# Kernel tuning notes

Measured on AMD Instinct MI355X. Metric: run time of the kernel, lower is better.

## Reference

```python
import jax, jax.numpy as jnp
import numpy as np

B, DIM, X, Y = 2, 256, 48, 48
HEADS, DIM_HEAD = 8, 64
DIM_INNER = HEADS * DIM_HEAD
MASK_SELF_VALUE = -100.0
EPS = 1e-12


def setup_inputs() -> dict:
    key = jax.random.key(0)
    k0, k1, k2, k3, k4 = jax.random.split(key, 5)
    return {
        "fmap": jax.random.normal(k0, (B, DIM, X, Y), dtype=jnp.float32),
        "gamma": jnp.ones((DIM,), dtype=jnp.float32),
        "w_qk": jax.random.normal(k1, (DIM_INNER, DIM), dtype=jnp.float32) * 0.02,
        "w_v": jax.random.normal(k2, (DIM_INNER, DIM), dtype=jnp.float32) * 0.02,
        "null_kv": jax.random.normal(k3, (2, HEADS, DIM_HEAD), dtype=jnp.float32),
        "w_out": jax.random.normal(k4, (DIM, DIM_INNER), dtype=jnp.float32) * 0.02,
    }


def _safe_sqrt(d2):
    # matches torch.cdist subgradient: zero grad at zero distance
    pos = d2 > 0
    return jnp.where(pos, jnp.sqrt(jnp.where(pos, d2, 1.0)), 0.0)


def reference(fmap, gamma, w_qk, w_v, null_kv, w_out):
    b, c, x, y = fmap.shape
    h, dh = HEADS, DIM_HEAD
    n = x * y
    scale = dh ** -0.5

    # ChannelRMSNorm: L2-normalize over channel dim, * sqrt(dim) * gamma
    l2 = jnp.sqrt(jnp.sum(fmap * fmap, axis=1, keepdims=True))
    normed = fmap / jnp.maximum(l2, EPS) * jnp.sqrt(jnp.float32(c)) * gamma[None, :, None, None]

    flat = normed.reshape(b, c, n)                       # b c n
    qk = jnp.einsum('oc,bcn->bon', w_qk, flat)           # b (h d) n
    v = jnp.einsum('oc,bcn->bon', w_v, flat)
    qk = qk.reshape(b, h, dh, n).transpose(0, 1, 3, 2)   # b h n d
    v = v.reshape(b, h, dh, n).transpose(0, 1, 3, 2)

    nk = jnp.broadcast_to(null_kv[0][None, :, None, :], (b, h, 1, dh))
    nv = jnp.broadcast_to(null_kv[1][None, :, None, :], (b, h, 1, dh))
    q = qk
    k = jnp.concatenate([nk, qk], axis=2)                # b h (n+1) d
    vv = jnp.concatenate([nv, v], axis=2)

    # -cdist(q, k, p=2) * scale via squared-distance expansion
    q2 = jnp.sum(q * q, axis=-1)[..., :, None]           # b h n 1
    k2 = jnp.sum(k * k, axis=-1)[..., None, :]           # b h 1 n+1
    cross = jnp.einsum('bhid,bhjd->bhij', q, k)          # b h n n+1
    d2 = jnp.maximum(q2 + k2 - 2.0 * cross, 0.0)
    sim = -_safe_sqrt(d2) * scale

    # mask self: eye(n) left-padded by one (null token never masked)
    self_mask = jnp.eye(n, n + 1, k=1, dtype=bool)
    sim = jnp.where(self_mask, MASK_SELF_VALUE, sim)

    attn = jax.nn.softmax(sim, axis=-1)
    out = jnp.einsum('bhij,bhjd->bhid', attn, vv)        # b h n d
    out = out.transpose(0, 1, 3, 2).reshape(b, h * dh, x, y)
    return jnp.einsum('oc,bcxy->boxy', w_out, out)
```

## Files before the change

### kernel.cpp

```cpp
#include <hip/hip_runtime.h>
#include <math.h>

#define NPOS 2304
#define CC   256
#define DI   512
#define NT   36
#define SCALE 0.125f
#define MASKV -100.0f
#define NEGSL2E (-0.18033688011112042f)

typedef __attribute__((ext_vector_type(8))) short bf16x8;
typedef __attribute__((ext_vector_type(4))) float f32x4;
typedef unsigned short u16;
typedef unsigned int u32;

__device__ inline u16 f2bf(float f) {
    union { float f; unsigned int u; } v; v.f = f;
    return (u16)((v.u + 0x7fffu + ((v.u >> 16) & 1u)) >> 16);
}
__device__ inline float bf2f(u16 h) { return __uint_as_float(((u32)h) << 16); }

__device__ inline bf16x8 ld_x8(const u16* p) {
    union { bf16x8 v; uint2 d[2]; } u;
    u.d[0] = *(const uint2*)(p + 0);
    u.d[1] = *(const uint2*)(p + 4);
    return u.v;
}

__device__ __forceinline__ void gl16(const u16* g, u16* l) {
    __builtin_amdgcn_global_load_lds(
        (const __attribute__((address_space(1))) void*)g,
        (__attribute__((address_space(3))) void*)l, 16, 0, 0);
}

__global__ __launch_bounds__(256) void k_proj(const float* __restrict__ fmap,
                                              const float* __restrict__ gamma,
                                              const float* __restrict__ wqk,
                                              const float* __restrict__ wv,
                                              const float* __restrict__ wout,
                                              const float* __restrict__ null_kv,
                                              u16* __restrict__ qkh,
                                              u16* __restrict__ vt,
                                              float* __restrict__ sq,
                                              float* __restrict__ ndot,
                                              float* __restrict__ nk2b,
                                              u16* __restrict__ wo_hi,
                                              u16* __restrict__ wo_lo) {
    const int blk = blockIdx.x;
    if (blk >= 576) {
        const int idx = blk - 576;
#pragma unroll
        for (int it = 0; it < 2; ++it) {
            const int k = idx * 512 + (int)threadIdx.x + it * 256;
            if (k < 32768) {
                const float4 v = ((const float4*)wout)[k];
                ushort4 h4, l4;
                h4.x = f2bf(v.x); l4.x = f2bf(v.x - bf2f(h4.x));
                h4.y = f2bf(v.y); l4.y = f2bf(v.y - bf2f(h4.y));
                h4.z = f2bf(v.z); l4.z = f2bf(v.z - bf2f(h4.z));
                h4.w = f2bf(v.w); l4.w = f2bf(v.w - bf2f(h4.w));
                ((ushort4*)wo_hi)[k] = h4;
                ((ushort4*)wo_lo)[k] = l4;
            }
        }
        return;
    }
    const int xcd = blk & 7;
    const int r   = blk >> 3;
    const int bh  = xcd * 2 + (r & 1);
    const int b   = bh >> 3;
    const int oy  = bh & 7;
    const int n0  = (r >> 1) * 64;

    const int t  = threadIdx.x;
    const int w = t >> 6, lane = t & 63, mcol = lane & 15, quad = lane >> 4;
    const int tx = t & 63, ty = t >> 6;

    __shared__ u16 X[64][260];
    __shared__ float red[4][64];
    __shared__ float inv_s[64];
    __shared__ float gs[256];
    __shared__ float sqp[4][64], ndp[4][64];
    u16 (*Tt)[68] = (u16(*)[68])X;

    gs[t] = gamma[t];
    const float* fb = fmap + (size_t)b * CC * NPOS;
    float v64[64];
#pragma unroll
    for (int i = 0; i < 64; ++i)
        v64[i] = fb[(ty * 64 + i) * NPOS + n0 + tx];
    float s = 0.0f;
#pragma unroll
    for (int i = 0; i < 64; ++i) s += v64[i] * v64[i];
    red[ty][tx] = s;
    __syncthreads();
    if (t < 64) {
        const float tt = red[0][t] + red[1][t] + red[2][t] + red[3][t];
        inv_s[t] = 16.0f / fmaxf(sqrtf(tt), 1e-12f);
    }
    __syncthreads();
    const float iv = inv_s[tx];
#pragma unroll
    for (int i = 0; i < 64; i += 2) {
        const int c = ty * 64 + i;
        const float v0 = v64[i] * iv * gs[c];
        const float v1 = v64[i + 1] * iv * gs[c + 1];
        *(u32*)&X[tx][c] = (u32)f2bf(v0) | ((u32)f2bf(v1) << 16);
    }
    if (blk == 0 && t < 8) {
        float s2 = 0.0f;
#pragma unroll 8
        for (int d = 0; d < 64; ++d) { const float x = null_kv[t * 64 + d]; s2 += x * x; }
        nk2b[t] = s2;
    }
    __syncthreads();

    const size_t wroff = (size_t)(oy * 64 + w * 16 + mcol) * 256 + quad * 8;
    const float* wrq = wqk + wroff;
    const float* wrv = wv + wroff;

    f32x4 cq[4], cv[4];
#pragma unroll
    for (int nf = 0; nf < 4; ++nf) {
        cq[nf] = (f32x4){0.f, 0.f, 0.f, 0.f};
        cv[nf] = (f32x4){0.f, 0.f, 0.f, 0.f};
    }
#pragma unroll
    for (int kc = 0; kc < 8; ++kc) {
        const float4 qa = *(const float4*)&wrq[kc * 32];
        const float4 qb4 = *(const float4*)&wrq[kc * 32 + 4];
        const float4 va = *(const float4*)&wrv[kc * 32];
        const float4 vb4 = *(const float4*)&wrv[kc * 32 + 4];
        bf16x8 aq, av;
        aq[0] = f2bf(qa.x);  aq[1] = f2bf(qa.y);  aq[2] = f2bf(qa.z);  aq[3] = f2bf(qa.w);
        aq[4] = f2bf(qb4.x); aq[5] = f2bf(qb4.y); aq[6] = f2bf(qb4.z); aq[7] = f2bf(qb4.w);
        av[0] = f2bf(va.x);  av[1] = f2bf(va.y);  av[2] = f2bf(va.z);  av[3] = f2bf(va.w);
        av[4] = f2bf(vb4.x); av[5] = f2bf(vb4.y); av[6] = f2bf(vb4.z); av[7] = f2bf(vb4.w);
        bf16x8 xB[4];
#pragma unroll
        for (int nf = 0; nf < 4; ++nf)
            xB[nf] = ld_x8(&X[nf * 16 + mcol][kc * 32 + quad * 8]);
#pragma unroll
        for (int nf = 0; nf < 4; ++nf) {
            cq[nf] = __builtin_amdgcn_mfma_f32_16x16x32_bf16(aq, xB[nf], cq[nf], 0, 0, 0);
            cv[nf] = __builtin_amdgcn_mfma_f32_16x16x32_bf16(av, xB[nf], cv[nf], 0, 0, 0);
        }
    }
    __syncthreads();

    {
        const int h = oy;
        const float4 nk4 = *(const float4*)&null_kv[h * 64 + w * 16 + quad * 4];
        float sv[4], nd[4];
#pragma unroll
        for (int nf = 0; nf < 4; ++nf) {
            sv[nf] = cq[nf][0] * cq[nf][0] + cq[nf][1] * cq[nf][1] + cq[nf][2] * cq[nf][2] + cq[nf][3] * cq[nf][3];
            nd[nf] = cq[nf][0] * nk4.x + cq[nf][1] * nk4.y + cq[nf][2] * nk4.z + cq[nf][3] * nk4.w;
        }
#pragma unroll
        for (int mk = 16; mk <= 32; mk <<= 1)
#pragma unroll
            for (int nf = 0; nf < 4; ++nf) {
                sv[nf] += __shfl_xor(sv[nf], mk);
                nd[nf] += __shfl_xor(nd[nf], mk);
            }
        if (quad == 0) {
#pragma unroll
            for (int nf = 0; nf < 4; ++nf) {
                sqp[w][nf * 16 + mcol] = sv[nf];
                ndp[w][nf * 16 + mcol] = nd[nf];
            }
        }
#pragma unroll
        for (int nf = 0; nf < 4; ++nf) {
            ushort4 r4;
            r4.x = f2bf(cq[nf][0]); r4.y = f2bf(cq[nf][1]);
            r4.z = f2bf(cq[nf][2]); r4.w = f2bf(cq[nf][3]);
            *(ushort4*)&Tt[nf * 16 + mcol][w * 16 + quad * 4] = r4;
        }
        __syncthreads();
        {
            const int n = t >> 2, ds = (t & 3) * 16;
            const uint2 r0 = *(const uint2*)&Tt[n][ds + 0];
            const uint2 r1 = *(const uint2*)&Tt[n][ds + 4];
            const uint2 r2 = *(const uint2*)&Tt[n][ds + 8];
            const uint2 r3 = *(const uint2*)&Tt[n][ds + 12];
            u16* dst = qkh + (((size_t)bh) * NPOS + n0 + n) * 64 + ds;
            *(uint4*)&dst[0] = make_uint4(r0.x, r0.y, r1.x, r1.y);
            *(uint4*)&dst[8] = make_uint4(r2.x, r2.y, r3.x, r3.y);
        }
        if (t < 64) {
            sq  [((size_t)bh) * NPOS + n0 + t] = sqp[0][t] + sqp[1][t] + sqp[2][t] + sqp[3][t];
            ndot[((size_t)bh) * NPOS + n0 + t] = ndp[0][t] + ndp[1][t] + ndp[2][t] + ndp[3][t];
        }
    }
    __syncthreads();

    {
#pragma unroll
        for (int nf = 0; nf < 4; ++nf)
#pragma unroll
            for (int rr = 0; rr < 4; ++rr)
                Tt[w * 16 + quad * 4 + rr][nf * 16 + mcol] = f2bf(cv[nf][rr]);
        __syncthreads();
        {
            const int d = t >> 2, ks = t & 3;
            const uint2 a0 = *(const uint2*)&Tt[d][ks * 16 + 0];
            const uint2 a1 = *(const uint2*)&Tt[d][ks * 16 + 4];
            const uint2 a2 = *(const uint2*)&Tt[d][ks * 16 + 8];
            const uint2 a3 = *(const uint2*)&Tt[d][ks * 16 + 12];
            u16* vdst = vt + (size_t)bh * (72 * 64 * 32);
            const int kb = (n0 >> 5) + (ks >> 1);
            u16* p = &vdst[((size_t)kb * 64 + d) * 32 + (ks & 1) * 16];
            *(uint4*)&p[0] = make_uint4(a0.x, a0.y, a1.x, a1.y);
            *(uint4*)&p[8] = make_uint4(a2.x, a2.y, a3.x, a3.y);
        }
    }
}

template <int KS>
__global__ __launch_bounds__(256) void k_attn(const u16* __restrict__ qkh,
                                              const u16* __restrict__ vt,
                                              const float* __restrict__ null_kv,
                                              const float* __restrict__ nk2b,
                                              const float* __restrict__ sq,
                                              const float* __restrict__ ndot,
                                              u16* __restrict__ ih,
                                              u16* __restrict__ il,
                                              float* __restrict__ pO,
                                              float* __restrict__ pL) {
    const int blk = blockIdx.x;
    const int xcd = blk & 7;
    const int j = blk >> 3;
    const int bh = xcd * 2 + (j & 1);
    const int r2 = j >> 1;
    const int qt = (KS == 2) ? (r2 >> 1) : r2;
    const int kh = (KS == 2) ? (r2 & 1) : 0;
    const int q0 = qt * 64;
    const int b = bh >> 3, h = bh & 7;
    const int t = threadIdx.x;
    const int wave = t >> 6, lane = t & 63;
    const int mcol = lane & 15, quad = lane >> 4;

    const int kt0 = kh * 18;
    const int NTL = (KS == 2) ? 18 : 36;

    __shared__ __align__(16) u16 sm[20992];
    u16* Kls = sm;
    u16* Vls = sm + 8192;
    u16 (*Pt)[72] = (u16(*)[72])(sm + 16384 + wave * 1152);

    const u16* qbase = qkh + (size_t)bh * NPOS * 64;
    const u16* vbase = vt + (size_t)bh * (72 * 64 * 32);
    const float* sqb = sq + (size_t)bh * NPOS;

    const int q16 = q0 + wave * 16;
    const bf16x8 bq00 = *(const bf16x8*)&qbase[(q16 + mcol) * 64 + quad * 8];
    const bf16x8 bq01 = *(const bf16x8*)&qbase[(q16 + mcol) * 64 + 32 + quad * 8];
    const float q2 = sqb[q16 + mcol];
    const int ktm = q16 >> 6;
    const int nbm = (q16 >> 4) & 3;

    const int kbase0 = (wave * 16 + 0) * 64;
    const int kbase1 = (wave * 16 + 8) * 64;
    const int ksrc0 = (wave * 16 + 0 + (lane >> 3)) * 64 + ((lane & 7) ^ (lane >> 3)) * 8;
    const int ksrc1 = (wave * 16 + 8 + (lane >> 3)) * 64 + ((lane & 7) ^ (lane >> 3)) * 8;
    const int vldsb = wave * 512;
    const int vsrc = (wave * 16 + (lane >> 2)) * 32 + ((lane & 3) ^ ((lane >> 3) & 3)) * 8;

    const int m7 = mcol & 7;
    const int mv = (mcol >> 1) & 3;

    {
        const u16* kg = qbase + (size_t)kt0 * 4096;
        const u16* vg = vbase + (size_t)kt0 * 4096;
        gl16(kg + ksrc0, Kls + kbase0);
        gl16(kg + ksrc1, Kls + kbase1);
        gl16(vg + vsrc,        Vls + vldsb);
        gl16(vg + 2048 + vsrc, Vls + 2048 + vldsb);
    }

    const bf16x8 ones = {0x3F80, 0x3F80, 0x3F80, 0x3F80, 0x3F80, 0x3F80, 0x3F80, 0x3F80};

    f32x4 oacc[4];
#pragma unroll
    for (int nb = 0; nb < 4; ++nb) oacc[nb] = (f32x4){0.f, 0.f, 0.f, 0.f};
    f32x4 lsum = (f32x4){0.f, 0.f, 0.f, 0.f};

    int p = 0;
#pragma unroll 1
    for (int i = 0; i < NTL; ++i) {
        const int kt = kt0 + i;
        __syncthreads();
        float4 k2q[4];
#pragma unroll
        for (int nb = 0; nb < 4; ++nb)
            k2q[nb] = *(const float4*)&sqb[kt * 64 + nb * 16 + quad * 4];
        if (i + 1 < NTL) {
            const u16* kg = qbase + (size_t)(kt + 1) * 4096;
            const u16* vg = vbase + (size_t)(kt + 1) * 4096;
            const int bb = (p ^ 1) * 4096;
            gl16(kg + ksrc0, Kls + bb + kbase0);
            gl16(kg + ksrc1, Kls + bb + kbase1);
            gl16(vg + vsrc,        Vls + bb + vldsb);
            gl16(vg + 2048 + vsrc, Vls + bb + 2048 + vldsb);
        }

        const u16* Kb = Kls + p * 4096;
        const u16* Vb = Vls + p * 4096;

        bf16x8 bk[4][2];
#pragma unroll
        for (int nb = 0; nb < 4; ++nb) {
            const int rr = (nb * 16 + mcol) * 64;
            bk[nb][0] = *(const bf16x8*)&Kb[rr + ((quad ^ m7)) * 8];
            bk[nb][1] = *(const bf16x8*)&Kb[rr + (((4 + quad) ^ m7)) * 8];
        }

        f32x4 c[4];
#pragma unroll
        for (int nb = 0; nb < 4; ++nb) {
            c[nb] = (f32x4){0.f, 0.f, 0.f, 0.f};
            c[nb] = __builtin_amdgcn_mfma_f32_16x16x32_bf16(bk[nb][0], bq00, c[nb], 0, 0, 0);
            c[nb] = __builtin_amdgcn_mfma_f32_16x16x32_bf16(bk[nb][1], bq01, c[nb], 0, 0, 0);
        }

        bf16x8 bv[4][2];
#pragma unroll
        for (int nb = 0; nb < 4; ++nb) {
            const int rr = (nb * 16 + mcol) * 32 + ((quad ^ mv)) * 8;
            bv[nb][0] = *(const bf16x8*)&Vb[rr];
            bv[nb][1] = *(const bf16x8*)&Vb[2048 + rr];
        }

#pragma unroll
        for (int nb = 0; nb < 4; ++nb) {
            float e[4];
#pragma unroll
            for (int r = 0; r < 4; ++r) {
                const float pre = q2 + ((const float*)&k2q[nb])[r];
                const float d2 = fmaxf(__builtin_fmaf(c[nb][r], -2.0f, pre), 0.0f);
                e[r] = __builtin_amdgcn_exp2f(NEGSL2E * __builtin_amdgcn_sqrtf(d2));
            }
            if (kt == ktm && nb == nbm) {
#pragma unroll
                for (int r = 0; r < 4; ++r)
                    if (quad * 4 + r == mcol) e[r] = 0.0f;
            }
            const u32 p01 = __builtin_amdgcn_perm(__float_as_uint(e[1]), __float_as_uint(e[0]), 0x07060302u);
            const u32 p23 = __builtin_amdgcn_perm(__float_as_uint(e[3]), __float_as_uint(e[2]), 0x07060302u);
            *(uint2*)&Pt[mcol][nb * 16 + quad * 4] = make_uint2(p01, p23);
        }

        const bf16x8 bp00 = *(const bf16x8*)&Pt[mcol][quad * 8];
        const bf16x8 bp01 = *(const bf16x8*)&Pt[mcol][32 + quad * 8];

#pragma unroll
        for (int nb = 0; nb < 4; ++nb) {
            oacc[nb] = __builtin_amdgcn_mfma_f32_16x16x32_bf16(bv[nb][0], bp00, oacc[nb], 0, 0, 0);
            oacc[nb] = __builtin_amdgcn_mfma_f32_16x16x32_bf16(bv[nb][1], bp01, oacc[nb], 0, 0, 0);
        }
        lsum = __builtin_amdgcn_mfma_f32_16x16x32_bf16(ones, bp00, lsum, 0, 0, 0);
        lsum = __builtin_amdgcn_mfma_f32_16x16x32_bf16(ones, bp01, lsum, 0, 0, 0);

        p ^= 1;
    }

    __syncthreads();

    float* Ofin = (float*)sm + wave * (16 * 68);
#pragma unroll
    for (int nb = 0; nb < 4; ++nb)
        *(f32x4*)&Ofin[mcol * 68 + nb * 16 + quad * 4] = oacc[nb];
    if (quad == 0) Ofin[mcol * 68 + 64] = lsum[0];

    {
        const int q = lane >> 2;
        const int d0 = (lane & 3) * 16;
        const float4 a0 = *(const float4*)&Ofin[q * 68 + d0 + 0];
        const float4 a1 = *(const float4*)&Ofin[q * 68 + d0 + 4];
        const float4 a2 = *(const float4*)&Ofin[q * 68 + d0 + 8];
        const float4 a3 = *(const float4*)&Ofin[q * 68 + d0 + 12];
        const float l = Ofin[q * 68 + 64];
        const int qg = q16 + q;

        if (KS == 2) {
            float* dst = pO + (size_t)kh * 2359296 + ((size_t)bh * NPOS + qg) * 64 + d0;
            *(float4*)&dst[0]  = a0;
            *(float4*)&dst[4]  = a1;
            *(float4*)&dst[8]  = a2;
            *(float4*)&dst[12] = a3;
            if ((lane & 3) == 0)
                pL[(size_t)kh * 36864 + (size_t)bh * NPOS + qg] = l;
        } else {
            const float q2v = sqb[qg];
            const float nd = ndot[(size_t)bh * NPOS + qg];
            const float nk2 = nk2b[h];
            const float d2n = fmaxf(q2v + nk2 - 2.0f * nd, 0.0f);
            const float beta = __expf(-sqrtf(d2n) * SCALE);
            const float ilv = 1.0f / (l + beta);

            const float* nvp = &null_kv[DI + h * 64 + d0];
            const float4 nv0 = *(const float4*)&nvp[0];
            const float4 nv1 = *(const float4*)&nvp[4];
            const float4 nv2 = *(const float4*)&nvp[8];
            const float4 nv3 = *(const float4*)&nvp[12];

            const size_t ob = ((size_t)b * NPOS + qg) * DI + h * 64 + d0;
            float vv[16];
            vv[0]  = (a0.x + beta * nv0.x) * ilv; vv[1]  = (a0.y + beta * nv0.y) * ilv;
            vv[2]  = (a0.z + beta * nv0.z) * ilv; vv[3]  = (a0.w + beta * nv0.w) * ilv;
            vv[4]  = (a1.x + beta * nv1.x) * ilv; vv[5]  = (a1.y + beta * nv1.y) * ilv;
            vv[6]  = (a1.z + beta * nv1.z) * ilv; vv[7]  = (a1.w + beta * nv1.w) * ilv;
            vv[8]  = (a2.x + beta * nv2.x) * ilv; vv[9]  = (a2.y + beta * nv2.y) * ilv;
            vv[10] = (a2.z + beta * nv2.z) * ilv; vv[11] = (a2.w + beta * nv2.w) * ilv;
            vv[12] = (a3.x + beta * nv3.x) * ilv; vv[13] = (a3.y + beta * nv3.y) * ilv;
            vv[14] = (a3.z + beta * nv3.z) * ilv; vv[15] = (a3.w + beta * nv3.w) * ilv;
#pragma unroll
            for (int g = 0; g < 4; ++g) {
                ushort4 hi4, lo4;
                hi4.x = f2bf(vv[g * 4 + 0]); lo4.x = f2bf(vv[g * 4 + 0] - bf2f(hi4.x));
                hi4.y = f2bf(vv[g * 4 + 1]); lo4.y = f2bf(vv[g * 4 + 1] - bf2f(hi4.y));
                hi4.z = f2bf(vv[g * 4 + 2]); lo4.z = f2bf(vv[g * 4 + 2] - bf2f(hi4.z));
                hi4.w = f2bf(vv[g * 4 + 3]); lo4.w = f2bf(vv[g * 4 + 3] - bf2f(hi4.w));
                *(ushort4*)&ih[ob + g * 4] = hi4;
                *(ushort4*)&il[ob + g * 4] = lo4;
            }
        }
    }
}

__global__ __launch_bounds__(256) void k_merge(const float* __restrict__ pO,
                                               const float* __restrict__ pL,
                                               const float* __restrict__ null_kv,
                                               const float* __restrict__ nk2b,
                                               const float* __restrict__ sq,
                                               const float* __restrict__ ndot,
                                               u16* __restrict__ ih,
                                               u16* __restrict__ il) {
    const int gid = blockIdx.x * 256 + (int)threadIdx.x;
    const int d0 = (gid & 3) * 16;
    const int t2 = gid >> 2;
    const int bh = t2 / NPOS;
    const int qg = t2 - bh * NPOS;
    const int b = bh >> 3, h = bh & 7;

    const size_t o0 = ((size_t)bh * NPOS + qg) * 64 + d0;
    const size_t o1 = o0 + 2359296;
    const float4 a0 = *(const float4*)&pO[o0 + 0];
    const float4 a1 = *(const float4*)&pO[o0 + 4];
    const float4 a2 = *(const float4*)&pO[o0 + 8];
    const float4 a3 = *(const float4*)&pO[o0 + 12];
    const float4 c0 = *(const float4*)&pO[o1 + 0];
    const float4 c1 = *(const float4*)&pO[o1 + 4];
    const float4 c2 = *(const float4*)&pO[o1 + 8];
    const float4 c3 = *(const float4*)&pO[o1 + 12];
    const float l = pL[(size_t)bh * NPOS + qg] + pL[36864 + (size_t)bh * NPOS + qg];

    const float q2v = sq[(size_t)bh * NPOS + qg];
    const float nd = ndot[(size_t)bh * NPOS + qg];
    const float nk2 = nk2b[h];
    const float d2n = fmaxf(q2v + nk2 - 2.0f * nd, 0.0f);
    const float beta = __expf(-sqrtf(d2n) * SCALE);
    const float ilv = 1.0f / (l + beta);

    const float* nvp = &null_kv[DI + h * 64 + d0];
    const float4 nv0 = *(const float4*)&nvp[0];
    const float4 nv1 = *(const float4*)&nvp[4];
    const float4 nv2 = *(const float4*)&nvp[8];
    const float4 nv3 = *(const float4*)&nvp[12];

    float vv[16];
    vv[0]  = (a0.x + c0.x + beta * nv0.x) * ilv; vv[1]  = (a0.y + c0.y + beta * nv0.y) * ilv;
    vv[2]  = (a0.z + c0.z + beta * nv0.z) * ilv; vv[3]  = (a0.w + c0.w + beta * nv0.w) * ilv;
    vv[4]  = (a1.x + c1.x + beta * nv1.x) * ilv; vv[5]  = (a1.y + c1.y + beta * nv1.y) * ilv;
    vv[6]  = (a1.z + c1.z + beta * nv1.z) * ilv; vv[7]  = (a1.w + c1.w + beta * nv1.w) * ilv;
    vv[8]  = (a2.x + c2.x + beta * nv2.x) * ilv; vv[9]  = (a2.y + c2.y + beta * nv2.y) * ilv;
    vv[10] = (a2.z + c2.z + beta * nv2.z) * ilv; vv[11] = (a2.w + c2.w + beta * nv2.w) * ilv;
    vv[12] = (a3.x + c3.x + beta * nv3.x) * ilv; vv[13] = (a3.y + c3.y + beta * nv3.y) * ilv;
    vv[14] = (a3.z + c3.z + beta * nv3.z) * ilv; vv[15] = (a3.w + c3.w + beta * nv3.w) * ilv;

    const size_t ob = ((size_t)b * NPOS + qg) * DI + h * 64 + d0;
#pragma unroll
    for (int g = 0; g < 4; ++g) {
        ushort4 hi4, lo4;
        hi4.x = f2bf(vv[g * 4 + 0]); lo4.x = f2bf(vv[g * 4 + 0] - bf2f(hi4.x));
        hi4.y = f2bf(vv[g * 4 + 1]); lo4.y = f2bf(vv[g * 4 + 1] - bf2f(hi4.y));
        hi4.z = f2bf(vv[g * 4 + 2]); lo4.z = f2bf(vv[g * 4 + 2] - bf2f(hi4.z));
        hi4.w = f2bf(vv[g * 4 + 3]); lo4.w = f2bf(vv[g * 4 + 3] - bf2f(hi4.w));
        *(ushort4*)&ih[ob + g * 4] = hi4;
        *(ushort4*)&il[ob + g * 4] = lo4;
    }
}

__global__ __launch_bounds__(256) void k_out(const u16* __restrict__ wo_hi,
                                             const u16* __restrict__ wo_lo,
                                             const u16* __restrict__ ih,
                                             const u16* __restrict__ il,
                                             float* __restrict__ out) {
    const int j0 = blockIdx.x * 32;
    const int c0 = blockIdx.y * 64;
    const int b  = blockIdx.z;
    const int t  = threadIdx.x;
    const int w = t >> 6, lane = t & 63, mcol = lane & 15, quad = lane >> 4;

    const u16* ah = wo_hi + (size_t)(c0 + w * 16 + mcol) * 512 + quad * 8;
    const u16* al = wo_lo + (size_t)(c0 + w * 16 + mcol) * 512 + quad * 8;
    const u16* xh = ih + ((size_t)b * NPOS + j0 + mcol) * 512 + quad * 8;
    const u16* xl = il + ((size_t)b * NPOS + j0 + mcol) * 512 + quad * 8;

    f32x4 c[2];
#pragma unroll
    for (int nf = 0; nf < 2; ++nf) c[nf] = (f32x4){0.f, 0.f, 0.f, 0.f};
#pragma unroll
    for (int kc = 0; kc < 16; ++kc) {
        const bf16x8 A  = *(const bf16x8*)&ah[kc * 32];
        const bf16x8 Al = *(const bf16x8*)&al[kc * 32];
        bf16x8 Bh[2], Bl[2];
#pragma unroll
        for (int nf = 0; nf < 2; ++nf) {
            Bh[nf] = *(const bf16x8*)&xh[(size_t)nf * 16 * 512 + kc * 32];
            Bl[nf] = *(const bf16x8*)&xl[(size_t)nf * 16 * 512 + kc * 32];
        }
#pragma unroll
        for (int nf = 0; nf < 2; ++nf) {
            c[nf] = __builtin_amdgcn_mfma_f32_16x16x32_bf16(A,  Bh[nf], c[nf], 0, 0, 0);
            c[nf] = __builtin_amdgcn_mfma_f32_16x16x32_bf16(A,  Bl[nf], c[nf], 0, 0, 0);
            c[nf] = __builtin_amdgcn_mfma_f32_16x16x32_bf16(Al, Bh[nf], c[nf], 0, 0, 0);
        }
    }
    float* ob = out + ((size_t)b * CC + c0 + w * 16) * NPOS + j0;
#pragma unroll
    for (int nf = 0; nf < 2; ++nf)
#pragma unroll
        for (int r = 0; r < 4; ++r)
            ob[(size_t)(quad * 4 + r) * NPOS + nf * 16 + mcol] = c[nf][r];
}

extern "C" void kernel_launch(void* const* d_in, const int* in_sizes, int n_in,
                              void* d_out, int out_size, void* d_ws, size_t ws_size,
                              hipStream_t stream) {
    const float* fmap    = (const float*)d_in[0];
    const float* gamma   = (const float*)d_in[1];
    const float* w_qk    = (const float*)d_in[2];
    const float* w_v     = (const float*)d_in[3];
    const float* null_kv = (const float*)d_in[4];
    const float* w_out   = (const float*)d_in[5];
    float* out = (float*)d_out;

    u16* ws16 = (u16*)d_ws;
    u16* qkh    = ws16;
    u16* vtb    = qkh + 2359296;
    u16* in_hi  = vtb + 2359296;
    u16* in_lo  = in_hi + 2359296;
    u16* wo_hi  = in_lo + 2359296;
    u16* wo_lo  = wo_hi + 131072;
    float* sqbuf = (float*)(wo_lo + 131072);
    float* ndbuf = sqbuf + 36864;
    float* nk2b  = ndbuf + 36864;
    float* pOws  = nk2b + 8;
    float* pLws  = pOws + 4718592;
    const size_t need_split = (size_t)((char*)(pLws + 73728) - (char*)d_ws);

    hipLaunchKernelGGL(k_proj, dim3(648),       dim3(256), 0, stream,
                       fmap, gamma, w_qk, w_v, w_out, null_kv, qkh, vtb, sqbuf, ndbuf, nk2b, wo_hi, wo_lo);
    if (ws_size >= need_split) {
        hipLaunchKernelGGL(HIP_KERNEL_NAME(k_attn<2>), dim3(1152), dim3(256), 0, stream,
                           qkh, vtb, null_kv, nk2b, sqbuf, ndbuf, in_hi, in_lo, pOws, pLws);
        hipLaunchKernelGGL(k_merge, dim3(576),  dim3(256), 0, stream,
                           pOws, pLws, null_kv, nk2b, sqbuf, ndbuf, in_hi, in_lo);
    } else {
        hipLaunchKernelGGL(HIP_KERNEL_NAME(k_attn<1>), dim3(576), dim3(256), 0, stream,
                           qkh, vtb, null_kv, nk2b, sqbuf, ndbuf, in_hi, in_lo, pOws, pLws);
    }
    hipLaunchKernelGGL(k_out,  dim3(72, 4, 2),  dim3(256), 0, stream,
                       wo_hi, wo_lo, in_hi, in_lo, out);
}
```

Baseline: 178.6 us.

## Pre-convert projection weights to bf16 and stage k_out B tiles through LDS

Adds a k_prep kernel that converts w_qk and w_v to bf16 once, along with the existing w_out hi/lo split, so k_proj loads bf16 weights directly instead of loading fp32 and converting in every block. k_out now stages the input hi/lo B tiles into double-buffered, XOR-swizzled LDS using global_load_lds, prefetching the next K phase while MFMAs run on the current one. This cuts redundant conversion work and uncoalesced global loads, at the cost of one extra kernel launch and more workspace.

```diff
diff --git a/kernel.cpp b/kernel.cpp
--- a/kernel.cpp
+++ b/kernel.cpp
@@ -33,38 +33,51 @@
         (__attribute__((address_space(3))) void*)l, 16, 0, 0);
 }
 
+__global__ __launch_bounds__(256) void k_prep(const float* __restrict__ wqk,
+                                              const float* __restrict__ wv,
+                                              const float* __restrict__ wout,
+                                              u16* __restrict__ wqkh,
+                                              u16* __restrict__ wvh,
+                                              u16* __restrict__ wo_hi,
+                                              u16* __restrict__ wo_lo) {
+    const int blk = blockIdx.x;
+    const int t = threadIdx.x;
+    if (blk < 128) {
+        const int k = blk * 256 + t;
+        const float4 v = ((const float4*)wqk)[k];
+        ushort4 h4;
+        h4.x = f2bf(v.x); h4.y = f2bf(v.y); h4.z = f2bf(v.z); h4.w = f2bf(v.w);
+        ((ushort4*)wqkh)[k] = h4;
+    } else if (blk < 256) {
+        const int k = (blk - 128) * 256 + t;
+        const float4 v = ((const float4*)wv)[k];
+        ushort4 h4;
+        h4.x = f2bf(v.x); h4.y = f2bf(v.y); h4.z = f2bf(v.z); h4.w = f2bf(v.w);
+        ((ushort4*)wvh)[k] = h4;
+    } else {
+        const int k = (blk - 256) * 256 + t;
+        const float4 v = ((const float4*)wout)[k];
+        ushort4 h4, l4;
+        h4.x = f2bf(v.x); l4.x = f2bf(v.x - bf2f(h4.x));
+        h4.y = f2bf(v.y); l4.y = f2bf(v.y - bf2f(h4.y));
+        h4.z = f2bf(v.z); l4.z = f2bf(v.z - bf2f(h4.z));
+        h4.w = f2bf(v.w); l4.w = f2bf(v.w - bf2f(h4.w));
+        ((ushort4*)wo_hi)[k] = h4;
+        ((ushort4*)wo_lo)[k] = l4;
+    }
+}
+
 __global__ __launch_bounds__(256) void k_proj(const float* __restrict__ fmap,
                                               const float* __restrict__ gamma,
-                                              const float* __restrict__ wqk,
-                                              const float* __restrict__ wv,
-                                              const float* __restrict__ wout,
+                                              const u16* __restrict__ wqkh,
+                                              const u16* __restrict__ wvh,
                                               const float* __restrict__ null_kv,
                                               u16* __restrict__ qkh,
                                               u16* __restrict__ vt,
                                               float* __restrict__ sq,
                                               float* __restrict__ ndot,
-                                              float* __restrict__ nk2b,
-                                              u16* __restrict__ wo_hi,
-                                              u16* __restrict__ wo_lo) {
+                                              float* __restrict__ nk2b) {
     const int blk = blockIdx.x;
-    if (blk >= 576) {
-        const int idx = blk - 576;
-#pragma unroll
-        for (int it = 0; it < 2; ++it) {
-            const int k = idx * 512 + (int)threadIdx.x + it * 256;
-            if (k < 32768) {
-                const float4 v = ((const float4*)wout)[k];
-                ushort4 h4, l4;
-                h4.x = f2bf(v.x); l4.x = f2bf(v.x - bf2f(h4.x));
-                h4.y = f2bf(v.y); l4.y = f2bf(v.y - bf2f(h4.y));
-                h4.z = f2bf(v.z); l4.z = f2bf(v.z - bf2f(h4.z));
-                h4.w = f2bf(v.w); l4.w = f2bf(v.w - bf2f(h4.w));
-                ((ushort4*)wo_hi)[k] = h4;
-                ((ushort4*)wo_lo)[k] = l4;
-            }
-        }
-        return;
-    }
     const int xcd = blk & 7;
     const int r   = blk >> 3;
     const int bh  = xcd * 2 + (r & 1);
@@ -116,8 +129,8 @@
     __syncthreads();
 
     const size_t wroff = (size_t)(oy * 64 + w * 16 + mcol) * 256 + quad * 8;
-    const float* wrq = wqk + wroff;
-    const float* wrv = wv + wroff;
+    const u16* wrq = wqkh + wroff;
+    const u16* wrv = wvh + wroff;
 
     f32x4 cq[4], cv[4];
 #pragma unroll
@@ -127,15 +140,8 @@
     }
 #pragma unroll
     for (int kc = 0; kc < 8; ++kc) {
-        const float4 qa = *(const float4*)&wrq[kc * 32];
-        const float4 qb4 = *(const float4*)&wrq[kc * 32 + 4];
-        const float4 va = *(const float4*)&wrv[kc * 32];
-        const float4 vb4 = *(const float4*)&wrv[kc * 32 + 4];
-        bf16x8 aq, av;
-        aq[0] = f2bf(qa.x);  aq[1] = f2bf(qa.y);  aq[2] = f2bf(qa.z);  aq[3] = f2bf(qa.w);
-        aq[4] = f2bf(qb4.x); aq[5] = f2bf(qb4.y); aq[6] = f2bf(qb4.z); aq[7] = f2bf(qb4.w);
-        av[0] = f2bf(va.x);  av[1] = f2bf(va.y);  av[2] = f2bf(va.z);  av[3] = f2bf(va.w);
-        av[4] = f2bf(vb4.x); av[5] = f2bf(vb4.y); av[6] = f2bf(vb4.z); av[7] = f2bf(vb4.w);
+        const bf16x8 aq = *(const bf16x8*)&wrq[kc * 32];
+        const bf16x8 av = *(const bf16x8*)&wrv[kc * 32];
         bf16x8 xB[4];
 #pragma unroll
         for (int nf = 0; nf < 4; ++nf)
@@ -504,30 +510,52 @@
     const int t  = threadIdx.x;
     const int w = t >> 6, lane = t & 63, mcol = lane & 15, quad = lane >> 4;
 
+    __shared__ __align__(16) u16 Bst[2][2][32][64];
+
     const u16* ah = wo_hi + (size_t)(c0 + w * 16 + mcol) * 512 + quad * 8;
     const u16* al = wo_lo + (size_t)(c0 + w * 16 + mcol) * 512 + quad * 8;
-    const u16* xh = ih + ((size_t)b * NPOS + j0 + mcol) * 512 + quad * 8;
-    const u16* xl = il + ((size_t)b * NPOS + j0 + mcol) * 512 + quad * 8;
+
+    const size_t bsrc_row = (size_t)b * NPOS + j0 + w * 8 + (lane >> 3);
+    const int bsg = ((lane & 7) ^ (lane >> 3)) * 8;
+    const u16* bsrc_h = ih + bsrc_row * 512 + bsg;
+    const u16* bsrc_l = il + bsrc_row * 512 + bsg;
+    u16* bdst_h = &Bst[0][0][w * 8][0];
+    u16* bdst_l = &Bst[0][1][w * 8][0];
+
+    gl16(bsrc_h, bdst_h);
+    gl16(bsrc_l, bdst_l);
 
     f32x4 c[2];
-#pragma unroll
-    for (int nf = 0; nf < 2; ++nf) c[nf] = (f32x4){0.f, 0.f, 0.f, 0.f};
-#pragma unroll
-    for (int kc = 0; kc < 16; ++kc) {
-        const bf16x8 A  = *(const bf16x8*)&ah[kc * 32];
-        const bf16x8 Al = *(const bf16x8*)&al[kc * 32];
-        bf16x8 Bh[2], Bl[2];
-#pragma unroll
-        for (int nf = 0; nf < 2; ++nf) {
-            Bh[nf] = *(const bf16x8*)&xh[(size_t)nf * 16 * 512 + kc * 32];
-            Bl[nf] = *(const bf16x8*)&xl[(size_t)nf * 16 * 512 + kc * 32];
-        }
-#pragma unroll
-        for (int nf = 0; nf < 2; ++nf) {
-            c[nf] = __builtin_amdgcn_mfma_f32_16x16x32_bf16(A,  Bh[nf], c[nf], 0, 0, 0);
-            c[nf] = __builtin_amdgcn_mfma_f32_16x16x32_bf16(A,  Bl[nf], c[nf], 0, 0, 0);
-            c[nf] = __builtin_amdgcn_mfma_f32_16x16x32_bf16(Al, Bh[nf], c[nf], 0, 0, 0);
-        }
+    c[0] = (f32x4){0.f, 0.f, 0.f, 0.f};
+    c[1] = (f32x4){0.f, 0.f, 0.f, 0.f};
+
+    int p = 0;
+#pragma unroll 1
+    for (int ph = 0; ph < 8; ++ph) {
+        __syncthreads();
+        if (ph + 1 < 8) {
+            const int ko = (ph + 1) * 64;
+            gl16(bsrc_h + ko, bdst_h + (p ^ 1) * 4096);
+            gl16(bsrc_l + ko, bdst_l + (p ^ 1) * 4096);
+        }
+        const u16* Bb = &Bst[p][0][0][0];
+#pragma unroll
+        for (int sub = 0; sub < 2; ++sub) {
+            const int kc = ph * 2 + sub;
+            const bf16x8 A  = *(const bf16x8*)&ah[kc * 32];
+            const bf16x8 Al = *(const bf16x8*)&al[kc * 32];
+#pragma unroll
+            for (int nf = 0; nf < 2; ++nf) {
+                const int r = nf * 16 + mcol;
+                const int g = (sub * 4 + quad) ^ (r & 7);
+                const bf16x8 Bh = *(const bf16x8*)&Bb[r * 64 + g * 8];
+                const bf16x8 Bl = *(const bf16x8*)&Bb[2048 + r * 64 + g * 8];
+                c[nf] = __builtin_amdgcn_mfma_f32_16x16x32_bf16(A,  Bh, c[nf], 0, 0, 0);
+                c[nf] = __builtin_amdgcn_mfma_f32_16x16x32_bf16(A,  Bl, c[nf], 0, 0, 0);
+                c[nf] = __builtin_amdgcn_mfma_f32_16x16x32_bf16(Al, Bh, c[nf], 0, 0, 0);
+            }
+        }
+        p ^= 1;
     }
     float* ob = out + ((size_t)b * CC + c0 + w * 16) * NPOS + j0;
 #pragma unroll
@@ -555,15 +583,19 @@
     u16* in_lo  = in_hi + 2359296;
     u16* wo_hi  = in_lo + 2359296;
     u16* wo_lo  = wo_hi + 131072;
-    float* sqbuf = (float*)(wo_lo + 131072);
+    u16* wqkh   = wo_lo + 131072;
+    u16* wvh    = wqkh + 131072;
+    float* sqbuf = (float*)(wvh + 131072);
     float* ndbuf = sqbuf + 36864;
     float* nk2b  = ndbuf + 36864;
     float* pOws  = nk2b + 8;
     float* pLws  = pOws + 4718592;
     const size_t need_split = (size_t)((char*)(pLws + 73728) - (char*)d_ws);
 
-    hipLaunchKernelGGL(k_proj, dim3(648),       dim3(256), 0, stream,
-                       fmap, gamma, w_qk, w_v, w_out, null_kv, qkh, vtb, sqbuf, ndbuf, nk2b, wo_hi, wo_lo);
+    hipLaunchKernelGGL(k_prep, dim3(384),       dim3(256), 0, stream,
+                       w_qk, w_v, w_out, wqkh, wvh, wo_hi, wo_lo);
+    hipLaunchKernelGGL(k_proj, dim3(576),       dim3(256), 0, stream,
+                       fmap, gamma, wqkh, wvh, null_kv, qkh, vtb, sqbuf, ndbuf, nk2b);
     if (ws_size >= need_split) {
         hipLaunchKernelGGL(HIP_KERNEL_NAME(k_attn<2>), dim3(1152), dim3(256), 0, stream,
                            qkh, vtb, null_kv, nk2b, sqbuf, ndbuf, in_hi, in_lo, pOws, pLws);
```

Measured after the change: 155.5 us, median of 2. -12.9%, faster.
